# Kernel tuning notes

Measured on AMD Instinct MI355X. Metric: run time of the kernel, lower is better.

Reference implementation:

```python
import jax, jax.numpy as jnp
import numpy as np

N_NODES = 100000
N_EDGES = 1250000
D_IN, D_HID, D_OUT = 64, 128, 64


def _seg_mean(msg, dst, n):
    # mean aggregation over incoming neighbors (PyG SAGEConv aggr='mean')
    s = jax.ops.segment_sum(msg, dst, num_segments=n)
    cnt = jax.ops.segment_sum(jnp.ones((msg.shape[0], 1), msg.dtype), dst, num_segments=n)
    return s / jnp.maximum(cnt, 1.0)


def setup_inputs() -> dict:
    key = jax.random.key(0)
    ks = jax.random.split(key, 8)
    x = jax.random.normal(ks[0], (N_NODES, D_IN), dtype=jnp.float32)
    edge_index = jax.random.randint(ks[1], (2, N_EDGES), 0, N_NODES, dtype=jnp.int32)
    # SAGEConv params: lin_l (on aggregated neighbors, with bias), lin_r (on root, no bias)
    s1 = 1.0 / np.sqrt(D_IN)
    s2 = 1.0 / np.sqrt(D_HID)
    W1_l = jax.random.normal(ks[2], (D_IN, D_HID), dtype=jnp.float32) * s1
    W1_r = jax.random.normal(ks[3], (D_IN, D_HID), dtype=jnp.float32) * s1
    b1 = jnp.zeros((D_HID,), dtype=jnp.float32)
    W2_l = jax.random.normal(ks[4], (D_HID, D_OUT), dtype=jnp.float32) * s2
    W2_r = jax.random.normal(ks[5], (D_HID, D_OUT), dtype=jnp.float32) * s2
    b2 = jnp.zeros((D_OUT,), dtype=jnp.float32)
    return {"x": x, "edge_index": edge_index, "W1_l": W1_l, "b1": b1, "W1_r": W1_r,
            "W2_l": W2_l, "b2": b2, "W2_r": W2_r}


def reference(x, edge_index, W1_l, b1, W1_r, W2_l, b2, W2_r):
    n = x.shape[0]
    src, dst = edge_index[0], edge_index[1]
    # layer 1: SAGEConv = lin_l(mean_{j in N(i)} x_j) + lin_r(x_i)
    agg1 = _seg_mean(x[src], dst, n)                      # [N, D_IN]
    h = agg1 @ W1_l + b1 + x @ W1_r                       # [N, D_HID]
    h = jax.nn.relu(h)                                    # dropout is identity in eval
    # layer 2
    agg2 = _seg_mean(h[src], dst, n)                      # [N, D_HID]
    out = agg2 @ W2_l + b2 + h @ W2_r                     # [N, D_OUT]
    return out
```

## Files before the change

kernel.cpp:

```cpp
#include <hip/hip_runtime.h>

#define NN 100000
#define NE 1250000

#define NBLK1 320
#define CHUNK 3907
#define NBUK  196
#define CAP   8192

typedef __attribute__((ext_vector_type(8))) short short8;
typedef __attribute__((ext_vector_type(4))) float f32x4;

static constexpr size_t I_BH    = 0;
static constexpr size_t I_BT    = 62720;
static constexpr size_t I_BB    = 62976;
static constexpr size_t I_OFFS  = 63232;
static constexpr size_t I_PAIRS = 163236;
static constexpr size_t I_SSRC  = 1413236;
static constexpr size_t U_BASE  = 5326472;
static constexpr size_t U_XB    = 0;
static constexpr size_t U_AGG   = 6400000;
static constexpr size_t U_P     = 12800000;
static constexpr size_t U_WF1   = 19200000;
static constexpr size_t U_WF2   = 19216384;

__device__ __forceinline__ float bf2f(unsigned int u16) {
    unsigned int v = u16 << 16;
    return __builtin_bit_cast(float, v);
}
__device__ __forceinline__ unsigned short f2bf(float f) {
    unsigned int u = __builtin_bit_cast(unsigned int, f);
    unsigned int r = (u + 0x7fffu + ((u >> 16) & 1u)) >> 16;
    return (unsigned short)r;
}

__global__ __launch_bounds__(256) void conv_x(const float* __restrict__ x,
                                              unsigned short* __restrict__ xb)
{
    int t = blockIdx.x * 256 + threadIdx.x;
    if (t >= NN * 16) return;
    float4 v = ((const float4*)x)[t];
    *(ushort4*)(xb + (size_t)t * 4) =
        make_ushort4(f2bf(v.x), f2bf(v.y), f2bf(v.z), f2bf(v.w));
}

__global__ __launch_bounds__(256) void prep_w(
    const float* __restrict__ W1l, const float* __restrict__ W1r,
    const float* __restrict__ W2l, const float* __restrict__ W2r,
    unsigned short* __restrict__ Wf1, unsigned short* __restrict__ Wf2)
{
    int i = blockIdx.x * 256 + threadIdx.x;
    if (i >= 16384) return;
    int e    = i & 7;
    int ch   = i >> 3;
    int lrow = ch & 15;
    int lk   = (ch >> 4) & 3;
    int kk   = (ch >> 6) & 3;
    int c    = ch >> 8;
    int j = c * 16 + lrow;
    int k = kk * 32 + lk * 8 + e;
    float w1 = (k < 64) ? W1l[(size_t)k * 128 + j] : W1r[(size_t)(k - 64) * 128 + j];
    Wf1[i] = f2bf(w1);
    float w2 = (j < 64) ? W2l[(size_t)k * 64 + j] : W2r[(size_t)k * 64 + (j - 64)];
    Wf2[i] = f2bf(w2);
}

__global__ __launch_bounds__(512) void p0_hist(const int* __restrict__ dstv,
                                               int* __restrict__ blockHist)
{
    __shared__ int hist[NBUK];
    const int t = threadIdx.x, b = blockIdx.x;
    for (int i = t; i < NBUK; i += 512) hist[i] = 0;
    __syncthreads();
    const int start = b * CHUNK;
    const int end   = min(start + CHUNK, NE);
    for (int e = start + t; e < end; e += 512)
        atomicAdd(&hist[dstv[e] >> 9], 1);
    __syncthreads();
    for (int i = t; i < NBUK; i += 512)
        blockHist[(size_t)i * NBLK1 + b] = hist[i];
}

__global__ __launch_bounds__(512) void p_scanA(int* __restrict__ blockHist,
                                               int* __restrict__ bucketTot)
{
    __shared__ int s[512];
    const int b = blockIdx.x, t = threadIdx.x;
    int v = (t < NBLK1) ? blockHist[(size_t)b * NBLK1 + t] : 0;
    s[t] = v;
    __syncthreads();
    for (int d = 1; d < 512; d <<= 1) {
        int x = (t >= d) ? s[t - d] : 0;
        __syncthreads();
        s[t] += x;
        __syncthreads();
    }
    if (t < NBLK1) blockHist[(size_t)b * NBLK1 + t] = s[t] - v;
    if (t == NBLK1 - 1) bucketTot[b] = s[t];
}

__global__ __launch_bounds__(256) void p_scanB(const int* __restrict__ bucketTot,
                                               int* __restrict__ bucketBase,
                                               int* __restrict__ offs)
{
    __shared__ int s[256];
    const int t = threadIdx.x;
    int v = (t < NBUK) ? bucketTot[t] : 0;
    s[t] = v;
    __syncthreads();
    for (int d = 1; d < 256; d <<= 1) {
        int x = (t >= d) ? s[t - d] : 0;
        __syncthreads();
        s[t] += x;
        __syncthreads();
    }
    if (t < NBUK) bucketBase[t] = s[t] - v;
    if (t == 0) { bucketBase[NBUK] = NE; offs[NN] = NE; }
}

__global__ __launch_bounds__(512) void p1_scatter(
    const int* __restrict__ srcv, const int* __restrict__ dstv,
    const int* __restrict__ blockHist, const int* __restrict__ bucketBase,
    int* __restrict__ pairs)
{
    __shared__ int cur[NBUK];
    const int t = threadIdx.x, b = blockIdx.x;
    for (int i = t; i < NBUK; i += 512)
        cur[i] = bucketBase[i] + blockHist[(size_t)i * NBLK1 + b];
    __syncthreads();
    const int start = b * CHUNK;
    const int end   = min(start + CHUNK, NE);
    for (int e = start + t; e < end; e += 512) {
        int d = dstv[e], s = srcv[e];
        int pos = atomicAdd(&cur[d >> 9], 1);
        pairs[pos] = s | ((d & 511) << 17);
    }
}

__global__ __launch_bounds__(1024) void p2_sort(
    const int* __restrict__ pairs, const int* __restrict__ bucketBase,
    int* __restrict__ offs, int* __restrict__ ssrc)
{
    __shared__ int buf[CAP];
    __shared__ int hist[512];
    const int b = blockIdx.x, t = threadIdx.x;
    const int base = bucketBase[b];
    const int m    = bucketBase[b + 1] - base;
    const bool fits = (m <= CAP);

    if (t < 512) hist[t] = 0;
    __syncthreads();
    for (int i = t; i < m; i += 1024) {
        int v = pairs[base + i];
        if (fits) buf[i] = v;
        atomicAdd(&hist[v >> 17], 1);
    }
    __syncthreads();

    int ov = (t < 512) ? hist[t] : 0;
    __syncthreads();
    for (int d = 1; d < 512; d <<= 1) {
        int x = 0;
        if (t < 512 && t >= d) x = hist[t - d];
        __syncthreads();
        if (t < 512) hist[t] += x;
        __syncthreads();
    }
    int excl = 0;
    if (t < 512) excl = hist[t] - ov;
    __syncthreads();
    if (t < 512) {
        hist[t] = excl;
        int n = b * 512 + t;
        if (n < NN) offs[n] = base + excl;
    }
    __syncthreads();
    for (int i = t; i < m; i += 1024) {
        int v = fits ? buf[i] : pairs[base + i];
        int pos = atomicAdd(&hist[v >> 17], 1);
        ssrc[base + pos] = v & 0x1FFFF;
    }
}

template <int FUSE>
__global__ __launch_bounds__(256) void sage_gather(
    const int* __restrict__ offs, const int* __restrict__ ssrc,
    const unsigned short* __restrict__ feat,
    const float* __restrict__ b2,
    unsigned short* __restrict__ aggb, float* __restrict__ out)
{
    const int t = blockIdx.x * 256 + threadIdx.x;
    const int n    = t >> 4;
    const int l    = t & 15;
    const int epar = l >> 3;
    const int ch   = l & 7;
    const int e0 = offs[n], e1 = offs[n + 1];

    float acc[8];
    #pragma unroll
    for (int j = 0; j < 8; ++j) acc[j] = 0.f;

    for (int e = e0 + epar; e < e1; e += 2) {
        int s = ssrc[e];
        uint4 u = *(const uint4*)(feat + (size_t)s * 64 + ch * 8);
        acc[0] += bf2f(u.x & 0xffffu); acc[1] += bf2f(u.x >> 16);
        acc[2] += bf2f(u.y & 0xffffu); acc[3] += bf2f(u.y >> 16);
        acc[4] += bf2f(u.z & 0xffffu); acc[5] += bf2f(u.z >> 16);
        acc[6] += bf2f(u.w & 0xffffu); acc[7] += bf2f(u.w >> 16);
    }
    #pragma unroll
    for (int j = 0; j < 8; ++j) acc[j] += __shfl_xor(acc[j], 8);
    if (epar) return;

    const int dg = e1 - e0;
    const float inv = 1.0f / (float)(dg > 0 ? dg : 1);
    #pragma unroll
    for (int j = 0; j < 8; ++j) acc[j] *= inv;

    if (FUSE == 0) {
        uint4 o;
        o.x = (unsigned)f2bf(acc[0]) | ((unsigned)f2bf(acc[1]) << 16);
        o.y = (unsigned)f2bf(acc[2]) | ((unsigned)f2bf(acc[3]) << 16);
        o.z = (unsigned)f2bf(acc[4]) | ((unsigned)f2bf(acc[5]) << 16);
        o.w = (unsigned)f2bf(acc[6]) | ((unsigned)f2bf(acc[7]) << 16);
        *(uint4*)(aggb + (size_t)n * 64 + ch * 8) = o;
    } else {
        float* o = out + (size_t)n * 64 + ch * 8;
        float4 q0 = *(const float4*)(o);
        float4 q1 = *(const float4*)(o + 4);
        float4 c0 = *(const float4*)(b2 + ch * 8);
        float4 c1 = *(const float4*)(b2 + ch * 8 + 4);
        *(float4*)(o)     = make_float4(acc[0] + q0.x + c0.x, acc[1] + q0.y + c0.y,
                                        acc[2] + q0.z + c0.z, acc[3] + q0.w + c0.w);
        *(float4*)(o + 4) = make_float4(acc[4] + q1.x + c1.x, acc[5] + q1.y + c1.y,
                                        acc[6] + q1.z + c1.z, acc[7] + q1.w + c1.w);
    }
}

__global__ __launch_bounds__(256) void sage_fused(
    const unsigned short* __restrict__ agg, const unsigned short* __restrict__ xb,
    const unsigned short* __restrict__ Wf1, const unsigned short* __restrict__ Wf2,
    const float* __restrict__ b1,
    unsigned short* __restrict__ p, float* __restrict__ outq)
{
    __shared__ __align__(16) unsigned short sW1[16384];
    __shared__ __align__(16) unsigned short sW2[16384];
    __shared__ __align__(16) unsigned short sh[4][2048];

    const int tid  = threadIdx.x;
    const int lane = tid & 63;
    const int wid  = tid >> 6;
    const int lrow = lane & 15;
    const int lk   = lane >> 4;

    {
        const uint4* g1 = (const uint4*)Wf1;
        const uint4* g2 = (const uint4*)Wf2;
        uint4* s1 = (uint4*)sW1;
        uint4* s2 = (uint4*)sW2;
        #pragma unroll
        for (int i = 0; i < 8; ++i) {
            int idx = tid + i * 256;
            s1[idx] = g1[idx];
            s2[idx] = g2[idx];
        }
    }
    __syncthreads();

    const int rbase = blockIdx.x * 64 + wid * 16;
    int arow = rbase + lrow;
    if (arow >= NN) arow = NN - 1;

    short8 a1[4];
    #pragma unroll
    for (int kk = 0; kk < 4; ++kk) {
        int k0 = kk * 32 + lk * 8;
        const unsigned short* ap = (k0 < 64) ? (agg + (size_t)arow * 64 + k0)
                                             : (xb  + (size_t)arow * 64 + (k0 - 64));
        a1[kk] = *(const short8*)ap;
    }

    const int fragoff = (lk * 16 + lrow) * 8;

    f32x4 acc1[8];
    #pragma unroll
    for (int c = 0; c < 8; ++c) {
        acc1[c] = (f32x4){0.f, 0.f, 0.f, 0.f};
        #pragma unroll
        for (int kk = 0; kk < 4; ++kk) {
            short8 b = *(const short8*)(sW1 + fragoff + c * 2048 + kk * 512);
            acc1[c] = __builtin_amdgcn_mfma_f32_16x16x32_bf16(a1[kk], b, acc1[c], 0, 0, 0);
        }
    }

    unsigned short* myh = &sh[wid][0];
    #pragma unroll
    for (int c = 0; c < 8; ++c) {
        float bv = b1[c * 16 + lrow];
        int chbase = ((2 * c + (lrow >> 3)) * 16 + lk * 4) * 8 + (lrow & 7);
        #pragma unroll
        for (int ri = 0; ri < 4; ++ri) {
            float v = fmaxf(acc1[c][ri] + bv, 0.f);
            myh[chbase + ri * 8] = f2bf(v);
        }
    }

    short8 a2[4];
    #pragma unroll
    for (int kk = 0; kk < 4; ++kk)
        a2[kk] = *(const short8*)(myh + fragoff + kk * 512);

    f32x4 acc2[8];
    #pragma unroll
    for (int c = 0; c < 8; ++c) {
        acc2[c] = (f32x4){0.f, 0.f, 0.f, 0.f};
        #pragma unroll
        for (int kk = 0; kk < 4; ++kk) {
            short8 b = *(const short8*)(sW2 + fragoff + c * 2048 + kk * 512);
            acc2[c] = __builtin_amdgcn_mfma_f32_16x16x32_bf16(a2[kk], b, acc2[c], 0, 0, 0);
        }
    }

    #pragma unroll
    for (int c = 0; c < 8; ++c) {
        int col = c * 16 + lrow;
        #pragma unroll
        for (int ri = 0; ri < 4; ++ri) {
            int row = rbase + lk * 4 + ri;
            if (row >= NN) continue;
            if (col < 64) p[(size_t)row * 64 + col] = f2bf(acc2[c][ri]);
            else          outq[(size_t)row * 64 + (col - 64)] = acc2[c][ri];
        }
    }
}

extern "C" void kernel_launch(void* const* d_in, const int* in_sizes, int n_in,
                              void* d_out, int out_size, void* d_ws, size_t ws_size,
                              hipStream_t stream)
{
    const float* x    = (const float*)d_in[0];
    const int*   ei   = (const int*)d_in[1];
    const float* W1_l = (const float*)d_in[2];
    const float* b1   = (const float*)d_in[3];
    const float* W1_r = (const float*)d_in[4];
    const float* W2_l = (const float*)d_in[5];
    const float* b2   = (const float*)d_in[6];
    const float* W2_r = (const float*)d_in[7];

    float* out = (float*)d_out;
    int*   wi  = (int*)d_ws;

    const int* srcv = ei;
    const int* dstv = ei + NE;

    int* blockHist  = wi + I_BH;
    int* bucketTot  = wi + I_BT;
    int* bucketBase = wi + I_BB;
    int* offs       = wi + I_OFFS;
    int* pairs      = wi + I_PAIRS;
    int* ssrc       = wi + I_SSRC;
    unsigned short* ub  = (unsigned short*)d_ws + U_BASE;
    unsigned short* xb  = ub + U_XB;
    unsigned short* agg = ub + U_AGG;
    unsigned short* p   = ub + U_P;
    unsigned short* Wf1 = ub + U_WF1;
    unsigned short* Wf2 = ub + U_WF2;

    conv_x <<<(NN * 16) / 256, 256, 0, stream>>>(x, xb);
    prep_w <<<64, 256, 0, stream>>>(W1_l, W1_r, W2_l, W2_r, Wf1, Wf2);

    p0_hist   <<<NBLK1, 512, 0, stream>>>(dstv, blockHist);
    p_scanA   <<<NBUK, 512, 0, stream>>>(blockHist, bucketTot);
    p_scanB   <<<1, 256, 0, stream>>>(bucketTot, bucketBase, offs);
    p1_scatter<<<NBLK1, 512, 0, stream>>>(srcv, dstv, blockHist, bucketBase, pairs);
    p2_sort   <<<NBUK, 1024, 0, stream>>>(pairs, bucketBase, offs, ssrc);

    sage_gather<0><<<(NN * 16) / 256, 256, 0, stream>>>(offs, ssrc, xb, nullptr, agg, nullptr);

    sage_fused<<<(NN + 63) / 64, 256, 0, stream>>>(agg, xb, Wf1, Wf2, b1, p, out);

    sage_gather<1><<<(NN * 16) / 256, 256, 0, stream>>>(offs, ssrc, p, b2, nullptr, out);
}
```

Before: 154.3 us.

## Store bf16 node features as channel-planar slices to localize gather reads

Feature tensors (x in bf16, the layer-1 aggregate, and the layer-2 projected features) are stored as 8 planes of 8 channels each instead of row-major 64-wide rows. Gather blocks now each handle a single channel plane for 128 nodes, so each plane (1.6 MB) can stay resident in cache while random source rows are read. The cost is that the fused MFMA kernel's scalar stores to the projection output become strided across planes, and the edge list and offsets are reread once per plane.

Measured after the change: 200.5 us. 1.3x slower.

```diff
diff --git a/kernel.cpp b/kernel.cpp
--- a/kernel.cpp
+++ b/kernel.cpp
@@ -2,11 +2,13 @@
 
 #define NN 100000
 #define NE 1250000
+#define PLANE 800000
 
 #define NBLK1 320
 #define CHUNK 3907
 #define NBUK  196
 #define CAP   8192
+#define GNB   782
 
 typedef __attribute__((ext_vector_type(8))) short short8;
 typedef __attribute__((ext_vector_type(4))) float f32x4;
@@ -28,20 +30,25 @@
     unsigned int v = u16 << 16;
     return __builtin_bit_cast(float, v);
 }
-__device__ __forceinline__ unsigned short f2bf(float f) {
+__device__ __forceinline__ unsigned int f2bf(float f) {
     unsigned int u = __builtin_bit_cast(unsigned int, f);
-    unsigned int r = (u + 0x7fffu + ((u >> 16) & 1u)) >> 16;
-    return (unsigned short)r;
+    return (u + 0x7fffu + ((u >> 16) & 1u)) >> 16;
 }
 
 __global__ __launch_bounds__(256) void conv_x(const float* __restrict__ x,
-                                              unsigned short* __restrict__ xb)
+                                              unsigned short* __restrict__ xbT)
 {
     int t = blockIdx.x * 256 + threadIdx.x;
-    if (t >= NN * 16) return;
-    float4 v = ((const float4*)x)[t];
-    *(ushort4*)(xb + (size_t)t * 4) =
-        make_ushort4(f2bf(v.x), f2bf(v.y), f2bf(v.z), f2bf(v.w));
+    if (t >= NN * 8) return;
+    int n = t >> 3, c = t & 7;
+    float4 v0 = *(const float4*)(x + (size_t)n * 64 + c * 8);
+    float4 v1 = *(const float4*)(x + (size_t)n * 64 + c * 8 + 4);
+    uint4 o;
+    o.x = f2bf(v0.x) | (f2bf(v0.y) << 16);
+    o.y = f2bf(v0.z) | (f2bf(v0.w) << 16);
+    o.z = f2bf(v1.x) | (f2bf(v1.y) << 16);
+    o.w = f2bf(v1.z) | (f2bf(v1.w) << 16);
+    *(uint4*)(xbT + (size_t)c * PLANE + (size_t)n * 8) = o;
 }
 
 __global__ __launch_bounds__(256) void prep_w(
@@ -185,32 +192,36 @@
 template <int FUSE>
 __global__ __launch_bounds__(256) void sage_gather(
     const int* __restrict__ offs, const int* __restrict__ ssrc,
-    const unsigned short* __restrict__ feat,
+    const unsigned short* __restrict__ featT,
     const float* __restrict__ b2,
-    unsigned short* __restrict__ aggb, float* __restrict__ out)
-{
-    const int t = blockIdx.x * 256 + threadIdx.x;
-    const int n    = t >> 4;
-    const int l    = t & 15;
-    const int epar = l >> 3;
-    const int ch   = l & 7;
+    unsigned short* __restrict__ aggT, float* __restrict__ out)
+{
+    const int b   = blockIdx.x;
+    const int c   = b & 7;
+    const int nb  = b >> 3;
+    const int tid = threadIdx.x;
+    const int nl  = tid >> 1;
+    const int par = tid & 1;
+    const int n   = nb * 128 + nl;
+    if (n >= NN) return;
     const int e0 = offs[n], e1 = offs[n + 1];
+    const unsigned short* plane = featT + (size_t)c * PLANE;
 
     float acc[8];
     #pragma unroll
     for (int j = 0; j < 8; ++j) acc[j] = 0.f;
 
-    for (int e = e0 + epar; e < e1; e += 2) {
+    for (int e = e0 + par; e < e1; e += 2) {
         int s = ssrc[e];
-        uint4 u = *(const uint4*)(feat + (size_t)s * 64 + ch * 8);
+        uint4 u = *(const uint4*)(plane + (size_t)s * 8);
         acc[0] += bf2f(u.x & 0xffffu); acc[1] += bf2f(u.x >> 16);
         acc[2] += bf2f(u.y & 0xffffu); acc[3] += bf2f(u.y >> 16);
         acc[4] += bf2f(u.z & 0xffffu); acc[5] += bf2f(u.z >> 16);
         acc[6] += bf2f(u.w & 0xffffu); acc[7] += bf2f(u.w >> 16);
     }
     #pragma unroll
-    for (int j = 0; j < 8; ++j) acc[j] += __shfl_xor(acc[j], 8);
-    if (epar) return;
+    for (int j = 0; j < 8; ++j) acc[j] += __shfl_xor(acc[j], 1);
+    if (par) return;
 
     const int dg = e1 - e0;
     const float inv = 1.0f / (float)(dg > 0 ? dg : 1);
@@ -219,17 +230,17 @@
 
     if (FUSE == 0) {
         uint4 o;
-        o.x = (unsigned)f2bf(acc[0]) | ((unsigned)f2bf(acc[1]) << 16);
-        o.y = (unsigned)f2bf(acc[2]) | ((unsigned)f2bf(acc[3]) << 16);
-        o.z = (unsigned)f2bf(acc[4]) | ((unsigned)f2bf(acc[5]) << 16);
-        o.w = (unsigned)f2bf(acc[6]) | ((unsigned)f2bf(acc[7]) << 16);
-        *(uint4*)(aggb + (size_t)n * 64 + ch * 8) = o;
+        o.x = f2bf(acc[0]) | (f2bf(acc[1]) << 16);
+        o.y = f2bf(acc[2]) | (f2bf(acc[3]) << 16);
+        o.z = f2bf(acc[4]) | (f2bf(acc[5]) << 16);
+        o.w = f2bf(acc[6]) | (f2bf(acc[7]) << 16);
+        *(uint4*)(aggT + (size_t)c * PLANE + (size_t)n * 8) = o;
     } else {
-        float* o = out + (size_t)n * 64 + ch * 8;
+        float* o = out + (size_t)n * 64 + c * 8;
         float4 q0 = *(const float4*)(o);
         float4 q1 = *(const float4*)(o + 4);
-        float4 c0 = *(const float4*)(b2 + ch * 8);
-        float4 c1 = *(const float4*)(b2 + ch * 8 + 4);
+        float4 c0 = *(const float4*)(b2 + c * 8);
+        float4 c1 = *(const float4*)(b2 + c * 8 + 4);
         *(float4*)(o)     = make_float4(acc[0] + q0.x + c0.x, acc[1] + q0.y + c0.y,
                                         acc[2] + q0.z + c0.z, acc[3] + q0.w + c0.w);
         *(float4*)(o + 4) = make_float4(acc[4] + q1.x + c1.x, acc[5] + q1.y + c1.y,
@@ -238,10 +249,10 @@
 }
 
 __global__ __launch_bounds__(256) void sage_fused(
-    const unsigned short* __restrict__ agg, const unsigned short* __restrict__ xb,
+    const unsigned short* __restrict__ aggT, const unsigned short* __restrict__ xbT,
     const unsigned short* __restrict__ Wf1, const unsigned short* __restrict__ Wf2,
     const float* __restrict__ b1,
-    unsigned short* __restrict__ p, float* __restrict__ outq)
+    unsigned short* __restrict__ pT, float* __restrict__ outq)
 {
     __shared__ __align__(16) unsigned short sW1[16384];
     __shared__ __align__(16) unsigned short sW2[16384];
@@ -275,8 +286,9 @@
     #pragma unroll
     for (int kk = 0; kk < 4; ++kk) {
         int k0 = kk * 32 + lk * 8;
-        const unsigned short* ap = (k0 < 64) ? (agg + (size_t)arow * 64 + k0)
-                                             : (xb  + (size_t)arow * 64 + (k0 - 64));
+        const unsigned short* ap = (k0 < 64)
+            ? (aggT + (size_t)(k0 >> 3) * PLANE + (size_t)arow * 8)
+            : (xbT  + (size_t)((k0 - 64) >> 3) * PLANE + (size_t)arow * 8);
         a1[kk] = *(const short8*)ap;
     }
 
@@ -328,8 +340,11 @@
         for (int ri = 0; ri < 4; ++ri) {
             int row = rbase + lk * 4 + ri;
             if (row >= NN) continue;
-            if (col < 64) p[(size_t)row * 64 + col] = f2bf(acc2[c][ri]);
-            else          outq[(size_t)row * 64 + (col - 64)] = acc2[c][ri];
+            if (col < 64)
+                pT[(size_t)(col >> 3) * PLANE + (size_t)row * 8 + (col & 7)] =
+                    f2bf(acc2[c][ri]);
+            else
+                outq[(size_t)row * 64 + (col - 64)] = acc2[c][ri];
         }
     }
 }
@@ -359,14 +374,14 @@
     int* offs       = wi + I_OFFS;
     int* pairs      = wi + I_PAIRS;
     int* ssrc       = wi + I_SSRC;
-    unsigned short* ub  = (unsigned short*)d_ws + U_BASE;
-    unsigned short* xb  = ub + U_XB;
-    unsigned short* agg = ub + U_AGG;
-    unsigned short* p   = ub + U_P;
-    unsigned short* Wf1 = ub + U_WF1;
-    unsigned short* Wf2 = ub + U_WF2;
-
-    conv_x <<<(NN * 16) / 256, 256, 0, stream>>>(x, xb);
+    unsigned short* ub   = (unsigned short*)d_ws + U_BASE;
+    unsigned short* xbT  = ub + U_XB;
+    unsigned short* aggT = ub + U_AGG;
+    unsigned short* pT   = ub + U_P;
+    unsigned short* Wf1  = ub + U_WF1;
+    unsigned short* Wf2  = ub + U_WF2;
+
+    conv_x <<<(NN * 8 + 255) / 256, 256, 0, stream>>>(x, xbT);
     prep_w <<<64, 256, 0, stream>>>(W1_l, W1_r, W2_l, W2_r, Wf1, Wf2);
 
     p0_hist   <<<NBLK1, 512, 0, stream>>>(dstv, blockHist);
@@ -375,9 +390,9 @@
     p1_scatter<<<NBLK1, 512, 0, stream>>>(srcv, dstv, blockHist, bucketBase, pairs);
     p2_sort   <<<NBUK, 1024, 0, stream>>>(pairs, bucketBase, offs, ssrc);
 
-    sage_gather<0><<<(NN * 16) / 256, 256, 0, stream>>>(offs, ssrc, xb, nullptr, agg, nullptr);
-
-    sage_fused<<<(NN + 63) / 64, 256, 0, stream>>>(agg, xb, Wf1, Wf2, b1, p, out);
-
-    sage_gather<1><<<(NN * 16) / 256, 256, 0, stream>>>(offs, ssrc, p, b2, nullptr, out);
-}
+    sage_gather<0><<<GNB * 8, 256, 0, stream>>>(offs, ssrc, xbT, nullptr, aggT, nullptr);
+
+    sage_fused<<<(NN + 63) / 64, 256, 0, stream>>>(aggT, xbT, Wf1, Wf2, b1, pT, out);
+
+    sage_gather<1><<<GNB * 8, 256, 0, stream>>>(offs, ssrc, pT, b2, nullptr, out);
+}
```
